# Kernel tuning notes

Measured on AMD Instinct MI355X. Metric: run time of the kernel, lower is better.

Reference implementation:

```python
import jax, jax.numpy as jnp
import numpy as np

N, E, G, H = 25000, 400000, 64, 8


def setup_inputs() -> dict:
    key = jax.random.key(0)
    ks = iter(jax.random.split(key, 64))
    nrm = lambda *s: jax.random.normal(next(ks), s, dtype=jnp.float32) * 0.1
    inp = {}
    inp['x'] = jax.random.normal(next(ks), (N, 3), dtype=jnp.float32)
    inp['edge_index'] = jax.random.randint(next(ks), (2, E), 0, N)
    inp['edge_attr'] = jax.random.uniform(next(ks), (E, 1), dtype=jnp.float32)
    inp['batch'] = jnp.sort(jax.random.randint(next(ks), (N,), 0, G))
    inp['inbn_g'] = jnp.ones(3, jnp.float32); inp['inbn_b'] = jnp.zeros(3, jnp.float32)
    # GAT layer 0: in=3, heads=8, C=8, concat -> 64
    inp['w0'] = nrm(3, 64); inp['we0'] = nrm(1, 64)
    inp['as0'] = nrm(8, 8); inp['ad0'] = nrm(8, 8); inp['ae0'] = nrm(8, 8)
    inp['b0'] = jnp.zeros(64, jnp.float32)
    inp['bng0'] = jnp.ones(64, jnp.float32); inp['bnb0'] = jnp.zeros(64, jnp.float32)
    # GAT layer 1: in=64, heads=8, C=8, concat -> 64
    inp['w1'] = nrm(64, 64); inp['we1'] = nrm(1, 64)
    inp['as1'] = nrm(8, 8); inp['ad1'] = nrm(8, 8); inp['ae1'] = nrm(8, 8)
    inp['b1'] = jnp.zeros(64, jnp.float32)
    inp['bng1'] = jnp.ones(64, jnp.float32); inp['bnb1'] = jnp.zeros(64, jnp.float32)
    # GAT layer 2: in=64, heads=8, C=64, concat=False (mean over heads) -> 64
    inp['w2'] = nrm(64, 512); inp['we2'] = nrm(1, 512)
    inp['as2'] = nrm(8, 64); inp['ad2'] = nrm(8, 64); inp['ae2'] = nrm(8, 64)
    inp['b2'] = jnp.zeros(64, jnp.float32)
    inp['bng2'] = jnp.ones(64, jnp.float32); inp['bnb2'] = jnp.zeros(64, jnp.float32)
    # MLP head (weights stored [in, out])
    inp['fc1_w'] = nrm(128, 128); inp['fc1_b'] = jnp.zeros(128, jnp.float32)
    inp['fc2_w'] = nrm(128, 64); inp['fc2_b'] = jnp.zeros(64, jnp.float32)
    inp['fg_w'] = nrm(64, 1); inp['fg_b'] = jnp.zeros(1, jnp.float32)
    inp['fb_w'] = nrm(64, 1); inp['fb_b'] = jnp.zeros(1, jnp.float32)
    return inp


def _bn(x, g, b):
    # training-mode batch norm over node dim (biased variance)
    m = x.mean(0)
    v = jnp.mean((x - m) ** 2, 0)
    return (x - m) * jax.lax.rsqrt(v + 1e-5) * g + b


def _gat(x, ei, ea, W, We, a_s, a_d, a_e, bias, concat):
    n = x.shape[0]
    h, c = a_s.shape
    xs = (x @ W).reshape(n, h, c)                       # [N,H,C]
    asrc = jnp.einsum('nhc,hc->nh', xs, a_s)            # [N,H]
    adst = jnp.einsum('nhc,hc->nh', xs, a_d)
    ee = (ea @ We).reshape(-1, h, c)                    # [E,H,C]
    aedge = jnp.einsum('ehc,hc->eh', ee, a_e)           # [E,H]
    s, d = ei[0], ei[1]
    logit = jax.nn.leaky_relu(asrc[s] + adst[d] + aedge, 0.2)   # [E,H]
    # segment softmax over incoming edges of each destination node
    mx = jax.ops.segment_max(logit, d, num_segments=n)
    mx = jnp.where(jnp.isfinite(mx), mx, 0.0)
    ez = jnp.exp(logit - mx[d])
    den = jax.ops.segment_sum(ez, d, num_segments=n)
    alpha = ez / jnp.maximum(den[d], 1e-16)             # [E,H]
    out = jax.ops.segment_sum(alpha[:, :, None] * xs[s], d, num_segments=n)  # [N,H,C]
    out = out.reshape(n, h * c) if concat else out.mean(1)
    return out + bias


def reference(x, edge_index, edge_attr, batch, inbn_g, inbn_b,
              w0, we0, as0, ad0, ae0, b0, bng0, bnb0,
              w1, we1, as1, ad1, ae1, b1, bng1, bnb1,
              w2, we2, as2, ad2, ae2, b2, bng2, bnb2,
              fc1_w, fc1_b, fc2_w, fc2_b, fg_w, fg_b, fb_w, fb_b):
    x = _bn(x, inbn_g, inbn_b)
    # layer 0 (no residual: 3 != 64)
    x = jax.nn.elu(_bn(_gat(x, edge_index, edge_attr, w0, we0, as0, ad0, ae0, b0, True), bng0, bnb0))
    # layer 1 (residual)
    x = x + jax.nn.elu(_bn(_gat(x, edge_index, edge_attr, w1, we1, as1, ad1, ae1, b1, True), bng1, bnb1))
    # layer 2 (concat=False, residual)
    x = x + jax.nn.elu(_bn(_gat(x, edge_index, edge_attr, w2, we2, as2, ad2, ae2, b2, False), bng2, bnb2))
    # dual pooling per graph
    cnt = jax.ops.segment_sum(jnp.ones((x.shape[0],), x.dtype), batch, num_segments=G)
    x_mean = jax.ops.segment_sum(x, batch, num_segments=G) / jnp.maximum(cnt, 1.0)[:, None]
    x_max = jax.ops.segment_max(x, batch, num_segments=G)
    g = jnp.concatenate([x_mean, x_max], axis=1)        # [G,128]
    g = jax.nn.elu(g @ fc1_w + fc1_b)
    g = jax.nn.elu(g @ fc2_w + fc2_b)
    gamma = g @ fg_w + fg_b
    beta = g @ fb_w + fb_b
    return jnp.concatenate([gamma, beta], axis=1)       # [G, 2*p_layers]
```

## Files before the change

### kernel.cpp

```cpp
#include <hip/hip_runtime.h>
#include <math.h>

#define NN 25000
#define EE 400000
#define GG 64
#define NB 64
#define PL 25024
#define EPB 6250

static const int O_CNT   = 0;
static const int O_ROWS  = 1601536;
static const int O_CUR   = 1626544;
static const int O_GOFF  = 3228080;
static const int O_IPART = 3228152;
static const int O_INBN  = 3228248;
static const int O_WS    = 3228256;
static const int O_WD    = 3229792;
static const int O_WE    = 3231328;
static const int O_BPART = 3231360;
static const int O_AB    = 3247744;
static const int O_BSW   = 3247872;
static const int O_CSRC  = 3264256;
static const int O_CEA   = 3664256;
static const int O_XS    = 4064256;
static const int O_ASRC  = 5664256;
static const int O_ADST  = 5864256;
static const int O_AGG   = 6064256;
static const int O_X     = 7664256;
static const int O_BSWC  = 9264256;
static const int O_BSWA  = 9266816;
static const int O_BSUM  = 9267328;
static const int O_BOFF  = 9267432;

using f32x4 = __attribute__((ext_vector_type(4))) float;
using sh8   = __attribute__((ext_vector_type(8))) short;

__device__ inline short f2bf(float f) {
    unsigned u = __float_as_uint(f);
    unsigned r = (u + 0x7FFFu + ((u >> 16) & 1u)) >> 16;
    return (short)r;
}

__global__ void k_pre(const int* __restrict__ batch, const float* __restrict__ x3,
                      const float* w0, const float* we0, const float* as0, const float* ad0, const float* ae0,
                      const float* w1, const float* we1, const float* as1, const float* ad1, const float* ae1,
                      const float* w2, const float* we2, const float* as2, const float* ad2, const float* ae2,
                      int* __restrict__ goff, float* __restrict__ ipart,
                      float* __restrict__ Ws, float* __restrict__ Wd, float* __restrict__ wev,
                      short* __restrict__ bsw, short* __restrict__ bswc, short* __restrict__ bswa) {
    __shared__ float sd[1536];
    int b = blockIdx.x, t = threadIdx.x;
    if (b < 16) {
        int ib = b;
        float s[3] = {0,0,0}, q[3] = {0,0,0};
        for (int n = ib * 256 + t; n < NN; n += 16 * 256) {
#pragma unroll
            for (int i = 0; i < 3; i++) { float v = x3[n*3+i]; s[i] += v; q[i] += v*v; }
        }
#pragma unroll
        for (int i = 0; i < 3; i++) { sd[t*6+i] = s[i]; sd[t*6+3+i] = q[i]; }
        __syncthreads();
        for (int off = 128; off > 0; off >>= 1) {
            if (t < off) {
#pragma unroll
                for (int i = 0; i < 6; i++) sd[t*6+i] += sd[(t+off)*6+i];
            }
            __syncthreads();
        }
        if (t < 6) ipart[ib*6 + t] = sd[t];
    } else if (b == 16) {
        if (t <= GG) {
            int g = t, lo = 0, hi = NN;
            while (lo < hi) { int mid = (lo + hi) >> 1; if (batch[mid] < g) lo = mid + 1; else hi = mid; }
            goff[g] = lo;
        }
    } else if (b < 20) {
        int L = b - 17;
        const float *W, *Wep, *as_, *ad_, *ae_; int INF, CC;
        if (L == 0)      { W = w0; Wep = we0; as_ = as0; ad_ = ad0; ae_ = ae0; INF = 3;  CC = 8;  }
        else if (L == 1) { W = w1; Wep = we1; as_ = as1; ad_ = ad1; ae_ = ae1; INF = 64; CC = 8;  }
        else             { W = w2; Wep = we2; as_ = as2; ad_ = ad2; ae_ = ae2; INF = 64; CC = 64; }
        int HC = 8 * CC;
        for (int tt = t; tt < INF * 8; tt += 256) {
            int i = tt >> 3, h = tt & 7;
            float s = 0.f, d = 0.f;
            for (int c = 0; c < CC; c++) {
                float w = W[i*HC + h*CC + c];
                s += w * as_[h*CC + c];
                d += w * ad_[h*CC + c];
            }
            Ws[L*512 + i*8 + h] = s; Wd[L*512 + i*8 + h] = d;
        }
        if (t < 8) {
            float s = 0.f;
            for (int c = 0; c < CC; c++) s += Wep[t*CC + c] * ae_[t*CC + c];
            wev[L*8 + t] = s;
        }
    } else if (b < 148) {
        int idx = (b - 20) * 256 + t;
        int j  = idx & 7;
        int l  = (idx >> 3) & 63;
        int nt = (idx >> 9) & 3;
        int kb = idx >> 11;
        int k = kb*32 + (l >> 4)*4 + (j & 3) + 16*(j >> 2);
        int c = nt*16 + (l & 15);
        int h = k >> 6, i = k & 63;
        bsw[idx] = f2bf(w2[i*512 + h*64 + c]);
    } else if (b < 168) {
        int idx = (b - 148) * 256 + t;
        int j  = idx & 7;
        int l  = (idx >> 3) & 63;
        int r2 = idx >> 9;
        int nt = r2 % 5, kb = r2 / 5;
        int k = kb*32 + (l >> 4)*4 + (j & 3) + 16*(j >> 2);
        int c = nt*16 + (l & 15);
        float val;
        if (c < 64) val = w1[k*64 + c];
        else {
            int h = (c - 64) & 7;
            const float* aa = (c < 72) ? as1 : ad1;
            float s = 0.f;
            for (int cc = 0; cc < 8; cc++) s += w1[k*64 + h*8 + cc] * aa[h*8 + cc];
            val = s;
        }
        bswc[idx] = f2bf(val);
    } else {
        int idx = (b - 168) * 256 + t;
        int j  = idx & 7;
        int l  = (idx >> 3) & 63;
        int kb = idx >> 9;
        int k = kb*32 + (l >> 4)*4 + (j & 3) + 16*(j >> 2);
        int c = l & 15;
        int h = c & 7;
        const float* aa = (c < 8) ? as2 : ad2;
        float s = 0.f;
        for (int cc = 0; cc < 64; cc++) s += w2[k*512 + h*64 + cc] * aa[h*64 + cc];
        bswa[idx] = f2bf(s);
    }
}

__global__ __launch_bounds__(256) void k_hist(const int* __restrict__ ei, int* __restrict__ cnt) {
    __shared__ int hb[PL];
    int t = threadIdx.x, b = blockIdx.x;
    for (int i = t; i < PL; i += 256) hb[i] = 0;
    __syncthreads();
    int e0 = b * EPB;
    for (int e = e0 + t; e < e0 + EPB; e += 256)
        atomicAdd(&hb[ei[EE + e]], 1);
    __syncthreads();
    for (int i = t; i < NN; i += 256) cnt[b * PL + i] = hb[i];
}

__global__ void k_scan1(const int* __restrict__ cnt, int* __restrict__ rows,
                        int* __restrict__ bsum) {
    int t = threadIdx.x, b = blockIdx.x;
    int i = b * 256 + t;
    int v = 0;
    if (i < NN) {
        for (int r = 0; r < NB; r++) v += cnt[r * PL + i];
    }
    __shared__ int sd[256];
    sd[t] = v; __syncthreads();
    for (int off = 1; off < 256; off <<= 1) {
        int x = (t >= off) ? sd[t - off] : 0;
        __syncthreads();
        sd[t] += x;
        __syncthreads();
    }
    if (i < NN) rows[i] = sd[t] - v;
    if (t == 255) bsum[b] = sd[255];
}

__global__ void k_scan2(const int* __restrict__ bsum, int* __restrict__ boff,
                        const float* __restrict__ ipart, float* __restrict__ inbn) {
    int t = threadIdx.x;
    if (t == 0) {
        int run = 0;
        for (int b = 0; b < 98; b++) { int v = bsum[b]; boff[b] = run; run += v; }
    }
    if (t < 6) { float s = 0.f; for (int b = 0; b < 16; b++) s += ipart[b*6 + t]; inbn[t] = s; }
}

__global__ void k_scan3(const int* __restrict__ boff, const int* __restrict__ cnt,
                        int* __restrict__ rows, int* __restrict__ cur) {
    int t = threadIdx.x, b = blockIdx.x;
    int i = b * 256 + t;
    if (i < NN) {
        int run = rows[i] + boff[b];
        rows[i] = run;
        for (int r = 0; r < NB; r++) {
            cur[r * PL + i] = run;
            run += cnt[r * PL + i];
        }
    }
    if (b == 0 && t == 0) rows[NN] = EE;
}

__global__ __launch_bounds__(256) void k_fill(const int* __restrict__ ei, const float* __restrict__ ea,
                       const int* __restrict__ cur, int* __restrict__ csrc,
                       float* __restrict__ cea) {
    __shared__ int lc[PL];
    int t = threadIdx.x, b = blockIdx.x;
    for (int i = t; i < NN; i += 256) lc[i] = cur[b * PL + i];
    __syncthreads();
    int e0 = b * EPB;
    for (int e = e0 + t; e < e0 + EPB; e += 256) {
        int s = ei[e], d = ei[EE + e];
        int pos = atomicAdd(&lc[d], 1);
        csrc[pos] = s; cea[pos] = ea[e];
    }
}

__global__ void k_proj0(const float* __restrict__ x, const float* __restrict__ sums,
                        const float* __restrict__ g, const float* __restrict__ b,
                        const float* __restrict__ W0,
                        const float* __restrict__ Ws, const float* __restrict__ Wd,
                        float* __restrict__ xs, float* __restrict__ asrc, float* __restrict__ adst) {
    int idx = blockIdx.x * 256 + threadIdx.x;
    if (idx >= NN * 64) return;
    int n = idx >> 6, j = idx & 63;
    float xn[3];
#pragma unroll
    for (int i = 0; i < 3; i++) {
        float m = sums[i] * (1.0f / NN);
        float v = sums[3+i] * (1.0f / NN) - m*m;
        xn[i] = (x[n*3+i] - m) * rsqrtf(v + 1e-5f) * g[i] + b[i];
    }
    float a = 0.f;
#pragma unroll
    for (int i = 0; i < 3; i++) a += xn[i] * W0[i*64 + j];
    xs[n*64 + j] = a;
    if (j < 16) {
        const float* WA = (j < 8) ? Ws : Wd;
        int h = j & 7;
        float s = 0.f;
#pragma unroll
        for (int i = 0; i < 3; i++) s += xn[i] * WA[i*8 + h];
        if (j < 8) asrc[n*8 + h] = s; else adst[n*8 + h] = s;
    }
}

__global__ void k_agg8f(const int* __restrict__ rows, const int* __restrict__ csrc,
                        const float* __restrict__ cea,
                        const float* __restrict__ asrc, const float* __restrict__ adst,
                        const float* __restrict__ wev,
                        const float* __restrict__ xs, float* __restrict__ agg) {
    int lane = threadIdx.x & 63;
    int d = (blockIdx.x * blockDim.x + threadIdx.x) >> 6;
    if (d >= NN) return;
    int h = lane >> 3;
    float adh = adst[d*8 + h];
    float wh  = wev[h];
    int rs = rows[d], re = rows[d+1];
    float acc = 0.f, den = 0.f;
    for (int c0 = rs; c0 < re; c0 += 64) {
        int cnt = re - c0; if (cnt > 64) cnt = 64;
        int ii = c0 + (lane < cnt ? lane : 0);
        int es = csrc[ii];
        float ef = cea[ii];
        int j = 0;
        for (; j + 3 < cnt; j += 4) {
            int s0 = __shfl(es, j),   s1 = __shfl(es, j+1);
            int s2 = __shfl(es, j+2), s3 = __shfl(es, j+3);
            float a0 = __shfl(ef, j),   a1 = __shfl(ef, j+1);
            float a2 = __shfl(ef, j+2), a3 = __shfl(ef, j+3);
            float l0 = asrc[s0*8+h], l1 = asrc[s1*8+h];
            float l2 = asrc[s2*8+h], l3 = asrc[s3*8+h];
            float x0 = xs[s0*64+lane], x1 = xs[s1*64+lane];
            float x2 = xs[s2*64+lane], x3 = xs[s3*64+lane];
            l0 += adh + a0*wh; l1 += adh + a1*wh;
            l2 += adh + a2*wh; l3 += adh + a3*wh;
            l0 = fmaxf(l0, 0.2f*l0); l1 = fmaxf(l1, 0.2f*l1);
            l2 = fmaxf(l2, 0.2f*l2); l3 = fmaxf(l3, 0.2f*l3);
            float e0 = __expf(l0), e1 = __expf(l1), e2 = __expf(l2), e3 = __expf(l3);
            den += (e0 + e1) + (e2 + e3);
            acc += e0*x0; acc += e1*x1; acc += e2*x2; acc += e3*x3;
        }
        for (; j < cnt; j++) {
            int s = __shfl(es, j);
            float a = __shfl(ef, j);
            float l = asrc[s*8+h] + adh + a*wh;
            l = fmaxf(l, 0.2f*l);
            float e = __expf(l);
            den += e;
            acc += e * xs[s*64+lane];
        }
    }
    agg[d*64 + lane] = acc / fmaxf(den, 1e-16f);
}

__global__ void k_proj1m(const float* __restrict__ agg, const float* __restrict__ ab,
                         const short* __restrict__ bswc,
                         float* __restrict__ xb, float* __restrict__ xs,
                         float* __restrict__ asrc, float* __restrict__ adst) {
    int l = threadIdx.x & 63;
    int wid = (blockIdx.x * blockDim.x + threadIdx.x) >> 6;
    int n0 = wid * 16;
    if (n0 >= NN) return;
    int ra = n0 + (l & 15); if (ra > NN-1) ra = NN-1;
    int kq = (l >> 4) * 4;
    const sh8* Bs = (const sh8*)bswc;
    sh8 af0, af1;
#pragma unroll
    for (int kb = 0; kb < 2; kb++) {
        int c0 = kb*32 + kq;
        float4 a0 = *(const float4*)&agg[ra*64 + c0];
        float4 a1 = *(const float4*)&agg[ra*64 + c0 + 16];
        float4 sc0 = *(const float4*)&ab[c0];
        float4 sh0 = *(const float4*)&ab[64 + c0];
        float4 sc1 = *(const float4*)&ab[c0 + 16];
        float4 sh1 = *(const float4*)&ab[64 + c0 + 16];
        float o[8];
        o[0] = a0.x*sc0.x + sh0.x; o[1] = a0.y*sc0.y + sh0.y;
        o[2] = a0.z*sc0.z + sh0.z; o[3] = a0.w*sc0.w + sh0.w;
        o[4] = a1.x*sc1.x + sh1.x; o[5] = a1.y*sc1.y + sh1.y;
        o[6] = a1.z*sc1.z + sh1.z; o[7] = a1.w*sc1.w + sh1.w;
#pragma unroll
        for (int u = 0; u < 8; u++) o[u] = (o[u] > 0.f) ? o[u] : (__expf(o[u]) - 1.f);
        float4 w0v = {o[0],o[1],o[2],o[3]}, w1v = {o[4],o[5],o[6],o[7]};
        *(float4*)&xb[ra*64 + c0]      = w0v;
        *(float4*)&xb[ra*64 + c0 + 16] = w1v;
        sh8 af;
#pragma unroll
        for (int u = 0; u < 8; u++) af[u] = f2bf(o[u]);
        if (kb == 0) af0 = af; else af1 = af;
    }
    f32x4 acc[5];
#pragma unroll
    for (int nt = 0; nt < 5; nt++) acc[nt] = (f32x4){0,0,0,0};
#pragma unroll
    for (int nt = 0; nt < 5; nt++) {
        acc[nt] = __builtin_amdgcn_mfma_f32_16x16x32_bf16(af0, Bs[nt*64 + l], acc[nt], 0, 0, 0);
        acc[nt] = __builtin_amdgcn_mfma_f32_16x16x32_bf16(af1, Bs[(5+nt)*64 + l], acc[nt], 0, 0, 0);
    }
    int rbase = n0 + (l >> 4) * 4, cb = l & 15;
#pragma unroll
    for (int r = 0; r < 4; r++) {
        int n = rbase + r;
        if (n >= NN) break;
#pragma unroll
        for (int nt = 0; nt < 4; nt++) xs[n*64 + nt*16 + cb] = acc[nt][r];
        if (cb < 8) asrc[n*8 + cb] = acc[4][r];
        else        adst[n*8 + (cb-8)] = acc[4][r];
    }
}

__global__ void k_bnattn(const float* __restrict__ agg, const float* __restrict__ ab,
                         const short* __restrict__ bswa,
                         float* __restrict__ xb,
                         float* __restrict__ asrc, float* __restrict__ adst) {
    int l = threadIdx.x & 63;
    int wid = (blockIdx.x * blockDim.x + threadIdx.x) >> 6;
    int n0 = wid * 16;
    if (n0 >= NN) return;
    int ra = n0 + (l & 15); if (ra > NN-1) ra = NN-1;
    int kq = (l >> 4) * 4;
    const sh8* Bs = (const sh8*)bswa;
    sh8 af0, af1;
#pragma unroll
    for (int kb = 0; kb < 2; kb++) {
        int c0 = kb*32 + kq;
        float4 a0 = *(const float4*)&agg[ra*64 + c0];
        float4 a1 = *(const float4*)&agg[ra*64 + c0 + 16];
        float4 x0 = *(const float4*)&xb[ra*64 + c0];
        float4 x1 = *(const float4*)&xb[ra*64 + c0 + 16];
        float4 sc0 = *(const float4*)&ab[c0];
        float4 sh0 = *(const float4*)&ab[64 + c0];
        float4 sc1 = *(const float4*)&ab[c0 + 16];
        float4 sh1 = *(const float4*)&ab[64 + c0 + 16];
        float o[8];
        o[0] = a0.x*sc0.x + sh0.x; o[1] = a0.y*sc0.y + sh0.y;
        o[2] = a0.z*sc0.z + sh0.z; o[3] = a0.w*sc0.w + sh0.w;
        o[4] = a1.x*sc1.x + sh1.x; o[5] = a1.y*sc1.y + sh1.y;
        o[6] = a1.z*sc1.z + sh1.z; o[7] = a1.w*sc1.w + sh1.w;
#pragma unroll
        for (int u = 0; u < 8; u++) o[u] = (o[u] > 0.f) ? o[u] : (__expf(o[u]) - 1.f);
        o[0] += x0.x; o[1] += x0.y; o[2] += x0.z; o[3] += x0.w;
        o[4] += x1.x; o[5] += x1.y; o[6] += x1.z; o[7] += x1.w;
        float4 w0v = {o[0],o[1],o[2],o[3]}, w1v = {o[4],o[5],o[6],o[7]};
        *(float4*)&xb[ra*64 + c0]      = w0v;
        *(float4*)&xb[ra*64 + c0 + 16] = w1v;
        sh8 af;
#pragma unroll
        for (int u = 0; u < 8; u++) af[u] = f2bf(o[u]);
        if (kb == 0) af0 = af; else af1 = af;
    }
    f32x4 acc = {0,0,0,0};
    acc = __builtin_amdgcn_mfma_f32_16x16x32_bf16(af0, Bs[l],      acc, 0, 0, 0);
    acc = __builtin_amdgcn_mfma_f32_16x16x32_bf16(af1, Bs[64 + l], acc, 0, 0, 0);
    int rbase = n0 + (l >> 4) * 4, cb = l & 15;
#pragma unroll
    for (int r = 0; r < 4; r++) {
        int n = rbase + r;
        if (n >= NN) break;
        if (cb < 8) asrc[n*8 + cb] = acc[r];
        else        adst[n*8 + (cb-8)] = acc[r];
    }
}

__global__ __launch_bounds__(1024) void k_l2f(
        const int* __restrict__ rows, const int* __restrict__ csrc,
        const float* __restrict__ cea,
        const float* __restrict__ asrc, const float* __restrict__ adst,
        const float* __restrict__ wev,
        const float* __restrict__ x, const short* __restrict__ bsw,
        float* __restrict__ agg) {
    __shared__ short zl[16 * 520];
    int t = threadIdx.x, lane = t & 63, wv = t >> 6;
    int blk = blockIdx.x;
    int h = lane >> 3;
    float wh = wev[h];
    const float4* x4 = (const float4*)x;
    int fo   = (lane & 7) * 2;
    int kb_w = lane >> 2;
    int qd0  = 2 * (lane & 1);
    int jhi  = 4 * ((lane >> 1) & 1);
    int r = wv;
    int d = blk * 16 + r;
    float acc[8] = {0,0,0,0,0,0,0,0};
    float den = 0.f;
    if (d < NN) {
        float adh = adst[d*8 + h];
        int rs = rows[d], re = rows[d+1];
        for (int c0 = rs; c0 < re; c0 += 64) {
            int cnt = re - c0; if (cnt > 64) cnt = 64;
            int ii = c0 + (lane < cnt ? lane : 0);
            int es = csrc[ii];
            float ef = cea[ii];
            int j = 0;
            for (; j + 1 < cnt; j += 2) {
                int s0 = __shfl(es, j), s1 = __shfl(es, j+1);
                float a0 = __shfl(ef, j), a1 = __shfl(ef, j+1);
                float l0 = asrc[s0*8+h], l1 = asrc[s1*8+h];
                float4 u0 = x4[s0*16 + fo], u1 = x4[s0*16 + fo + 1];
                float4 v0 = x4[s1*16 + fo], v1 = x4[s1*16 + fo + 1];
                l0 += adh + a0*wh; l1 += adh + a1*wh;
                l0 = fmaxf(l0, 0.2f*l0); l1 = fmaxf(l1, 0.2f*l1);
                float e0 = __expf(l0), e1 = __expf(l1);
                den += e0 + e1;
                acc[0] += e0*u0.x + e1*v0.x;
                acc[1] += e0*u0.y + e1*v0.y;
                acc[2] += e0*u0.z + e1*v0.z;
                acc[3] += e0*u0.w + e1*v0.w;
                acc[4] += e0*u1.x + e1*v1.x;
                acc[5] += e0*u1.y + e1*v1.y;
                acc[6] += e0*u1.z + e1*v1.z;
                acc[7] += e0*u1.w + e1*v1.w;
            }
            if (j < cnt) {
                int s = __shfl(es, j);
                float a = __shfl(ef, j);
                float l = asrc[s*8+h] + adh + a*wh;
                l = fmaxf(l, 0.2f*l);
                float e = __expf(l);
                den += e;
                float4 u0 = x4[s*16 + fo], u1 = x4[s*16 + fo + 1];
                acc[0] += e*u0.x; acc[1] += e*u0.y; acc[2] += e*u0.z; acc[3] += e*u0.w;
                acc[4] += e*u1.x; acc[5] += e*u1.y; acc[6] += e*u1.z; acc[7] += e*u1.w;
            }
        }
    }
    float inv = 1.0f / fmaxf(den, 1e-16f);
    short4 lo, hi;
    lo.x = f2bf(acc[0]*inv); lo.y = f2bf(acc[1]*inv);
    lo.z = f2bf(acc[2]*inv); lo.w = f2bf(acc[3]*inv);
    hi.x = f2bf(acc[4]*inv); hi.y = f2bf(acc[5]*inv);
    hi.z = f2bf(acc[6]*inv); hi.w = f2bf(acc[7]*inv);
    *(short4*)&zl[kb_w*520 + (r + 16*qd0)*8 + jhi]     = lo;
    *(short4*)&zl[kb_w*520 + (r + 16*(qd0+1))*8 + jhi] = hi;
    __syncthreads();
    if (wv < 4) {
        const sh8* Bs = (const sh8*)bsw;
        f32x4 oacc = {0,0,0,0};
        for (int kb = 0; kb < 16; kb++) {
            sh8 a = *(const sh8*)&zl[kb*520 + lane*8];
            sh8 bf = Bs[(kb*4 + wv)*64 + lane];
            oacc = __builtin_amdgcn_mfma_f32_16x16x32_bf16(a, bf, oacc, 0, 0, 0);
        }
        int row = blk*16 + (lane >> 4) * 4;
        int col = wv*16 + (lane & 15);
#pragma unroll
        for (int rr = 0; rr < 4; rr++) {
            int n = row + rr;
            if (n < NN) agg[(size_t)n*64 + col] = oacc[rr] * 0.125f;
        }
    }
}

__global__ void k_bnstats(const float* __restrict__ agg, float* __restrict__ part) {
    int t = threadIdx.x;
    int c = t & 63;
    int r0 = blockIdx.x * 4 + (t >> 6);
    float s = 0.f, q = 0.f;
    for (int n = r0; n < NN; n += gridDim.x * 4) {
        float y = agg[n*64 + c];
        s += y; q += y*y;
    }
    __shared__ float sd[512];
    sd[t] = s; sd[256 + t] = q;
    __syncthreads();
    if (t < 128) { sd[t] += sd[t+128]; sd[256+t] += sd[256+t+128]; }
    __syncthreads();
    if (t < 64) {
        part[blockIdx.x*128 + t]      = sd[t] + sd[t+64];
        part[blockIdx.x*128 + 64 + t] = sd[256+t] + sd[256+t+64];
    }
}

__global__ void k_bnfin(const float* __restrict__ part, const float* __restrict__ gam,
                        const float* __restrict__ bet, float* __restrict__ ab) {
    int c = threadIdx.x;
    if (c >= 64) return;
    float s = 0.f, q = 0.f;
    for (int b = 0; b < 128; b++) { s += part[b*128 + c]; q += part[b*128 + 64 + c]; }
    float m = s * (1.0f / NN);
    float v = q * (1.0f / NN) - m*m;
    float a = gam[c] * rsqrtf(v + 1e-5f);
    ab[c] = a;
    ab[64 + c] = bet[c] - m * a;
}

__global__ void k_poolmlp(const float* __restrict__ xb, const float* __restrict__ agg,
                          const float* __restrict__ ab, const int* __restrict__ goff,
                          const float* __restrict__ fc1w, const float* __restrict__ fc1b,
                          const float* __restrict__ fc2w, const float* __restrict__ fc2b,
                          const float* __restrict__ fgw, const float* __restrict__ fgb,
                          const float* __restrict__ fbw, const float* __restrict__ fbb,
                          float* __restrict__ out) {
    int g = blockIdx.x, t = threadIdx.x;
    int c = t & 63, r = t >> 6;
    float a = ab[c], sh = ab[64 + c];
    int st = goff[g], en = goff[g+1];
    float s = 0.f, mx = -INFINITY;
    for (int n = st + r; n < en; n += 4) {
        float o = agg[n*64 + c] * a + sh;
        o = (o > 0.f) ? o : (__expf(o) - 1.0f);
        float v = xb[n*64 + c] + o;
        s += v; mx = fmaxf(mx, v);
    }
    __shared__ float sd[512];
    __shared__ float sg[128], s1[128], s2[64];
    sd[t] = s; sd[256 + t] = mx;
    __syncthreads();
    if (t < 128) { sd[t] += sd[t+128]; sd[256+t] = fmaxf(sd[256+t], sd[256+t+128]); }
    __syncthreads();
    if (t < 64) {
        float cnt = (float)(en - st);
        sg[t]      = (sd[t] + sd[t+64]) / fmaxf(cnt, 1.0f);
        sg[64 + t] = fmaxf(sd[256+t], sd[256+t+64]);
    }
    __syncthreads();
    if (t < 128) {
        float av = fc1b[t];
        for (int i = 0; i < 128; i++) av += sg[i] * fc1w[i*128 + t];
        s1[t] = (av > 0.f) ? av : (__expf(av) - 1.f);
    }
    __syncthreads();
    if (t < 64) {
        float bv = fc2b[t];
        for (int i = 0; i < 128; i++) bv += s1[i] * fc2w[i*64 + t];
        s2[t] = (bv > 0.f) ? bv : (__expf(bv) - 1.f);
    }
    __syncthreads();
    if (t == 0) {
        float ga = fgb[0], be = fbb[0];
        for (int i = 0; i < 64; i++) { ga += s2[i] * fgw[i]; be += s2[i] * fbw[i]; }
        out[g*2 + 0] = ga;
        out[g*2 + 1] = be;
    }
}

extern "C" void kernel_launch(void* const* d_in, const int* in_sizes, int n_in,
                              void* d_out, int out_size, void* d_ws, size_t ws_size,
                              hipStream_t stream) {
    (void)in_sizes; (void)n_in; (void)out_size; (void)ws_size;
    const float* x3    = (const float*)d_in[0];
    const int*   ei    = (const int*)d_in[1];
    const float* ea    = (const float*)d_in[2];
    const int*   batch = (const int*)d_in[3];
    const float* ing   = (const float*)d_in[4];
    const float* inb   = (const float*)d_in[5];
    const float* w0    = (const float*)d_in[6];
    const float* we0   = (const float*)d_in[7];
    const float* as0   = (const float*)d_in[8];
    const float* ad0   = (const float*)d_in[9];
    const float* ae0   = (const float*)d_in[10];
    const float* bng0  = (const float*)d_in[12];
    const float* bnb0  = (const float*)d_in[13];
    const float* w1    = (const float*)d_in[14];
    const float* we1   = (const float*)d_in[15];
    const float* as1   = (const float*)d_in[16];
    const float* ad1   = (const float*)d_in[17];
    const float* ae1   = (const float*)d_in[18];
    const float* bng1  = (const float*)d_in[20];
    const float* bnb1  = (const float*)d_in[21];
    const float* w2    = (const float*)d_in[22];
    const float* we2   = (const float*)d_in[23];
    const float* as2   = (const float*)d_in[24];
    const float* ad2   = (const float*)d_in[25];
    const float* ae2   = (const float*)d_in[26];
    const float* bng2  = (const float*)d_in[28];
    const float* bnb2  = (const float*)d_in[29];
    const float* fc1w  = (const float*)d_in[30];
    const float* fc1b  = (const float*)d_in[31];
    const float* fc2w  = (const float*)d_in[32];
    const float* fc2b  = (const float*)d_in[33];
    const float* fgw   = (const float*)d_in[34];
    const float* fgb   = (const float*)d_in[35];
    const float* fbw   = (const float*)d_in[36];
    const float* fbb   = (const float*)d_in[37];

    float* fws = (float*)d_ws;
    int*   iws = (int*)d_ws;
    int*   cnt   = iws + O_CNT;
    int*   rows  = iws + O_ROWS;
    int*   cur   = iws + O_CUR;
    int*   goff  = iws + O_GOFF;
    float* ipart = fws + O_IPART;
    float* inbn  = fws + O_INBN;
    float* Ws    = fws + O_WS;
    float* Wd    = fws + O_WD;
    float* wev   = fws + O_WE;
    float* bpart = fws + O_BPART;
    float* ab    = fws + O_AB;
    short* bsw   = (short*)(fws + O_BSW);
    int*   csrc  = iws + O_CSRC;
    float* cea   = fws + O_CEA;
    float* xs    = fws + O_XS;
    float* asrc  = fws + O_ASRC;
    float* adst  = fws + O_ADST;
    float* agg   = fws + O_AGG;
    float* xb    = fws + O_X;
    short* bswc  = (short*)(fws + O_BSWC);
    short* bswa  = (short*)(fws + O_BSWA);
    int*   bsum  = iws + O_BSUM;
    int*   boff  = iws + O_BOFF;

    k_pre<<<172, 256, 0, stream>>>(batch, x3,
                                   w0, we0, as0, ad0, ae0,
                                   w1, we1, as1, ad1, ae1,
                                   w2, we2, as2, ad2, ae2,
                                   goff, ipart, Ws, Wd, wev, bsw, bswc, bswa);
    k_hist<<<NB, 256, 0, stream>>>(ei, cnt);
    k_scan1<<<98, 256, 0, stream>>>(cnt, rows, bsum);
    k_scan2<<<1, 64, 0, stream>>>(bsum, boff, ipart, inbn);
    k_scan3<<<98, 256, 0, stream>>>(boff, cnt, rows, cur);
    k_fill<<<NB, 256, 0, stream>>>(ei, ea, cur, csrc, cea);

    const int nblk64 = (NN * 64 + 255) / 256;
    const int wblk16 = ((NN + 15) / 16 + 3) / 4;

    k_proj0<<<nblk64, 256, 0, stream>>>(x3, inbn, ing, inb, w0, Ws, Wd, xs, asrc, adst);
    k_agg8f<<<nblk64, 256, 0, stream>>>(rows, csrc, cea, asrc, adst, wev, xs, agg);
    k_bnstats<<<128, 256, 0, stream>>>(agg, bpart);
    k_bnfin<<<1, 64, 0, stream>>>(bpart, bng0, bnb0, ab);

    k_proj1m<<<wblk16, 256, 0, stream>>>(agg, ab, bswc, xb, xs, asrc, adst);
    k_agg8f<<<nblk64, 256, 0, stream>>>(rows, csrc, cea, asrc, adst, wev + 8, xs, agg);
    k_bnstats<<<128, 256, 0, stream>>>(agg, bpart);
    k_bnfin<<<1, 64, 0, stream>>>(bpart, bng1, bnb1, ab);

    k_bnattn<<<wblk16, 256, 0, stream>>>(agg, ab, bswa, xb, asrc, adst);
    k_l2f<<<(NN + 15) / 16, 1024, 0, stream>>>(rows, csrc, cea, asrc, adst, wev + 16,
                                               xb, bsw, agg);
    k_bnstats<<<128, 256, 0, stream>>>(agg, bpart);
    k_bnfin<<<1, 64, 0, stream>>>(bpart, bng2, bnb2, ab);

    k_poolmlp<<<GG, 256, 0, stream>>>(xb, agg, ab, goff, fc1w, fc1b, fc2w, fc2b,
                                      fgw, fgb, fbw, fbb, (float*)d_out);
}
```

Baseline: 413.8 us.

## Store gathered node features in bf16 to halve edge-gather traffic

The projected node features read by the three edge-aggregation kernels are now written in bf16 instead of fp32, and a separate bf16 copy of the layer-2 input is produced in k_bnattn for k_l2f. Each edge gather then reads half as many bytes from random source rows, which targets the memory-bound aggregation loops. Accumulation stays in fp32. The trade-off is reduced precision in the aggregated features and an extra bf16 write in k_bnattn.

```diff
diff --git a/kernel.cpp b/kernel.cpp
--- a/kernel.cpp
+++ b/kernel.cpp
@@ -23,6 +23,7 @@
 static const int O_CSRC  = 3264256;
 static const int O_CEA   = 3664256;
 static const int O_XS    = 4064256;
+static const int O_XH    = 4864256;
 static const int O_ASRC  = 5664256;
 static const int O_ADST  = 5864256;
 static const int O_AGG   = 6064256;
@@ -39,6 +40,9 @@
     unsigned u = __float_as_uint(f);
     unsigned r = (u + 0x7FFFu + ((u >> 16) & 1u)) >> 16;
     return (short)r;
+}
+__device__ inline float bf2f(unsigned short u) {
+    return __uint_as_float(((unsigned)u) << 16);
 }
 
 __global__ void k_pre(const int* __restrict__ batch, const float* __restrict__ x3,
@@ -215,7 +219,8 @@
                         const float* __restrict__ g, const float* __restrict__ b,
                         const float* __restrict__ W0,
                         const float* __restrict__ Ws, const float* __restrict__ Wd,
-                        float* __restrict__ xs, float* __restrict__ asrc, float* __restrict__ adst) {
+                        unsigned short* __restrict__ xs16,
+                        float* __restrict__ asrc, float* __restrict__ adst) {
     int idx = blockIdx.x * 256 + threadIdx.x;
     if (idx >= NN * 64) return;
     int n = idx >> 6, j = idx & 63;
@@ -229,7 +234,7 @@
     float a = 0.f;
 #pragma unroll
     for (int i = 0; i < 3; i++) a += xn[i] * W0[i*64 + j];
-    xs[n*64 + j] = a;
+    xs16[n*64 + j] = (unsigned short)f2bf(a);
     if (j < 16) {
         const float* WA = (j < 8) ? Ws : Wd;
         int h = j & 7;
@@ -244,7 +249,7 @@
                         const float* __restrict__ cea,
                         const float* __restrict__ asrc, const float* __restrict__ adst,
                         const float* __restrict__ wev,
-                        const float* __restrict__ xs, float* __restrict__ agg) {
+                        const unsigned short* __restrict__ xs16, float* __restrict__ agg) {
     int lane = threadIdx.x & 63;
     int d = (blockIdx.x * blockDim.x + threadIdx.x) >> 6;
     if (d >= NN) return;
@@ -266,8 +271,8 @@
             float a2 = __shfl(ef, j+2), a3 = __shfl(ef, j+3);
             float l0 = asrc[s0*8+h], l1 = asrc[s1*8+h];
             float l2 = asrc[s2*8+h], l3 = asrc[s3*8+h];
-            float x0 = xs[s0*64+lane], x1 = xs[s1*64+lane];
-            float x2 = xs[s2*64+lane], x3 = xs[s3*64+lane];
+            float x0 = bf2f(xs16[s0*64+lane]), x1 = bf2f(xs16[s1*64+lane]);
+            float x2 = bf2f(xs16[s2*64+lane]), x3 = bf2f(xs16[s3*64+lane]);
             l0 += adh + a0*wh; l1 += adh + a1*wh;
             l2 += adh + a2*wh; l3 += adh + a3*wh;
             l0 = fmaxf(l0, 0.2f*l0); l1 = fmaxf(l1, 0.2f*l1);
@@ -283,7 +288,7 @@
             l = fmaxf(l, 0.2f*l);
             float e = __expf(l);
             den += e;
-            acc += e * xs[s*64+lane];
+            acc += e * bf2f(xs16[s*64+lane]);
         }
     }
     agg[d*64 + lane] = acc / fmaxf(den, 1e-16f);
@@ -291,7 +296,7 @@
 
 __global__ void k_proj1m(const float* __restrict__ agg, const float* __restrict__ ab,
                          const short* __restrict__ bswc,
-                         float* __restrict__ xb, float* __restrict__ xs,
+                         float* __restrict__ xb, unsigned short* __restrict__ xs16,
                          float* __restrict__ asrc, float* __restrict__ adst) {
     int l = threadIdx.x & 63;
     int wid = (blockIdx.x * blockDim.x + threadIdx.x) >> 6;
@@ -339,7 +344,8 @@
         int n = rbase + r;
         if (n >= NN) break;
 #pragma unroll
-        for (int nt = 0; nt < 4; nt++) xs[n*64 + nt*16 + cb] = acc[nt][r];
+        for (int nt = 0; nt < 4; nt++)
+            xs16[n*64 + nt*16 + cb] = (unsigned short)f2bf(acc[nt][r]);
         if (cb < 8) asrc[n*8 + cb] = acc[4][r];
         else        adst[n*8 + (cb-8)] = acc[4][r];
     }
@@ -347,7 +353,7 @@
 
 __global__ void k_bnattn(const float* __restrict__ agg, const float* __restrict__ ab,
                          const short* __restrict__ bswa,
-                         float* __restrict__ xb,
+                         float* __restrict__ xb, unsigned short* __restrict__ xh16,
                          float* __restrict__ asrc, float* __restrict__ adst) {
     int l = threadIdx.x & 63;
     int wid = (blockIdx.x * blockDim.x + threadIdx.x) >> 6;
@@ -380,6 +386,11 @@
         float4 w0v = {o[0],o[1],o[2],o[3]}, w1v = {o[4],o[5],o[6],o[7]};
         *(float4*)&xb[ra*64 + c0]      = w0v;
         *(float4*)&xb[ra*64 + c0 + 16] = w1v;
+        short4 h0, h1;
+        h0.x = f2bf(o[0]); h0.y = f2bf(o[1]); h0.z = f2bf(o[2]); h0.w = f2bf(o[3]);
+        h1.x = f2bf(o[4]); h1.y = f2bf(o[5]); h1.z = f2bf(o[6]); h1.w = f2bf(o[7]);
+        *(short4*)&xh16[ra*64 + c0]      = h0;
+        *(short4*)&xh16[ra*64 + c0 + 16] = h1;
         sh8 af;
 #pragma unroll
         for (int u = 0; u < 8; u++) af[u] = f2bf(o[u]);
@@ -403,15 +414,15 @@
         const float* __restrict__ cea,
         const float* __restrict__ asrc, const float* __restrict__ adst,
         const float* __restrict__ wev,
-        const float* __restrict__ x, const short* __restrict__ bsw,
+        const unsigned short* __restrict__ xh16, const short* __restrict__ bsw,
         float* __restrict__ agg) {
     __shared__ short zl[16 * 520];
     int t = threadIdx.x, lane = t & 63, wv = t >> 6;
     int blk = blockIdx.x;
     int h = lane >> 3;
     float wh = wev[h];
-    const float4* x4 = (const float4*)x;
-    int fo   = (lane & 7) * 2;
+    const sh8* xh8 = (const sh8*)xh16;
+    int fo8  = lane & 7;
     int kb_w = lane >> 2;
     int qd0  = 2 * (lane & 1);
     int jhi  = 4 * ((lane >> 1) & 1);
@@ -432,20 +443,15 @@
                 int s0 = __shfl(es, j), s1 = __shfl(es, j+1);
                 float a0 = __shfl(ef, j), a1 = __shfl(ef, j+1);
                 float l0 = asrc[s0*8+h], l1 = asrc[s1*8+h];
-                float4 u0 = x4[s0*16 + fo], u1 = x4[s0*16 + fo + 1];
-                float4 v0 = x4[s1*16 + fo], v1 = x4[s1*16 + fo + 1];
+                sh8 u8 = xh8[s0*8 + fo8];
+                sh8 v8 = xh8[s1*8 + fo8];
                 l0 += adh + a0*wh; l1 += adh + a1*wh;
                 l0 = fmaxf(l0, 0.2f*l0); l1 = fmaxf(l1, 0.2f*l1);
                 float e0 = __expf(l0), e1 = __expf(l1);
                 den += e0 + e1;
-                acc[0] += e0*u0.x + e1*v0.x;
-                acc[1] += e0*u0.y + e1*v0.y;
-                acc[2] += e0*u0.z + e1*v0.z;
-                acc[3] += e0*u0.w + e1*v0.w;
-                acc[4] += e0*u1.x + e1*v1.x;
-                acc[5] += e0*u1.y + e1*v1.y;
-                acc[6] += e0*u1.z + e1*v1.z;
-                acc[7] += e0*u1.w + e1*v1.w;
+#pragma unroll
+                for (int u = 0; u < 8; u++)
+                    acc[u] += e0 * bf2f((unsigned short)u8[u]) + e1 * bf2f((unsigned short)v8[u]);
             }
             if (j < cnt) {
                 int s = __shfl(es, j);
@@ -454,9 +460,10 @@
                 l = fmaxf(l, 0.2f*l);
                 float e = __expf(l);
                 den += e;
-                float4 u0 = x4[s*16 + fo], u1 = x4[s*16 + fo + 1];
-                acc[0] += e*u0.x; acc[1] += e*u0.y; acc[2] += e*u0.z; acc[3] += e*u0.w;
-                acc[4] += e*u1.x; acc[5] += e*u1.y; acc[6] += e*u1.z; acc[7] += e*u1.w;
+                sh8 u8 = xh8[s*8 + fo8];
+#pragma unroll
+                for (int u = 0; u < 8; u++)
+                    acc[u] += e * bf2f((unsigned short)u8[u]);
             }
         }
     }
@@ -626,7 +633,8 @@
     short* bsw   = (short*)(fws + O_BSW);
     int*   csrc  = iws + O_CSRC;
     float* cea   = fws + O_CEA;
-    float* xs    = fws + O_XS;
+    unsigned short* xs16 = (unsigned short*)(fws + O_XS);
+    unsigned short* xh16 = (unsigned short*)(fws + O_XH);
     float* asrc  = fws + O_ASRC;
     float* adst  = fws + O_ADST;
     float* agg   = fws + O_AGG;
@@ -650,19 +658,19 @@
     const int nblk64 = (NN * 64 + 255) / 256;
     const int wblk16 = ((NN + 15) / 16 + 3) / 4;
 
-    k_proj0<<<nblk64, 256, 0, stream>>>(x3, inbn, ing, inb, w0, Ws, Wd, xs, asrc, adst);
-    k_agg8f<<<nblk64, 256, 0, stream>>>(rows, csrc, cea, asrc, adst, wev, xs, agg);
+    k_proj0<<<nblk64, 256, 0, stream>>>(x3, inbn, ing, inb, w0, Ws, Wd, xs16, asrc, adst);
+    k_agg8f<<<nblk64, 256, 0, stream>>>(rows, csrc, cea, asrc, adst, wev, xs16, agg);
     k_bnstats<<<128, 256, 0, stream>>>(agg, bpart);
     k_bnfin<<<1, 64, 0, stream>>>(bpart, bng0, bnb0, ab);
 
-    k_proj1m<<<wblk16, 256, 0, stream>>>(agg, ab, bswc, xb, xs, asrc, adst);
-    k_agg8f<<<nblk64, 256, 0, stream>>>(rows, csrc, cea, asrc, adst, wev + 8, xs, agg);
+    k_proj1m<<<wblk16, 256, 0, stream>>>(agg, ab, bswc, xb, xs16, asrc, adst);
+    k_agg8f<<<nblk64, 256, 0, stream>>>(rows, csrc, cea, asrc, adst, wev + 8, xs16, agg);
     k_bnstats<<<128, 256, 0, stream>>>(agg, bpart);
     k_bnfin<<<1, 64, 0, stream>>>(bpart, bng1, bnb1, ab);
 
-    k_bnattn<<<wblk16, 256, 0, stream>>>(agg, ab, bswa, xb, asrc, adst);
+    k_bnattn<<<wblk16, 256, 0, stream>>>(agg, ab, bswa, xb, xh16, asrc, adst);
     k_l2f<<<(NN + 15) / 16, 1024, 0, stream>>>(rows, csrc, cea, asrc, adst, wev + 16,
-                                               xb, bsw, agg);
+                                               xh16, bsw, agg);
     k_bnstats<<<128, 256, 0, stream>>>(agg, bpart);
     k_bnfin<<<1, 64, 0, stream>>>(bpart, bng2, bnb2, ab);
 
```

New measurement: 408.2 us. Within noise of the previous version (-1.4%).
